# Kernel optimization log

Measured on AMD Instinct MI355X. Metric: run time of the kernel, lower is better.

Reference implementation:

```python
import jax, jax.numpy as jnp
import numpy as np

TOP_K = 8
N_GROUP = 8
TOPK_GROUP = 4
ROUTED_SCALE = 2.5


def setup_inputs() -> dict:
    key = jax.random.key(0)
    ks = jax.random.split(key, 7)
    T, H, E, I, SI = 4096, 1024, 32, 512, 2048
    W = 0.05  # weight scale to keep relu^2 activations sane
    return {
        "hidden_states": jax.random.normal(ks[0], (T, H), jnp.float32),
        "gate_w": jax.random.normal(ks[1], (E, H), jnp.float32) * W,
        "bias": jax.random.normal(ks[2], (E,), jnp.float32),
        "w_up": jax.random.normal(ks[3], (E, I, H), jnp.float32) * W,
        "w_down": jax.random.normal(ks[4], (E, H, I), jnp.float32) * W,
        "shared_up": jax.random.normal(ks[5], (SI, H), jnp.float32) * W,
        "shared_down": jax.random.normal(ks[6], (H, SI), jnp.float32) * W,
    }


def _grouped_topk_sigmoid(logits, bias):
    # vLLM grouped_topk with scoring_func='sigmoid' + e_score_correction_bias
    T, E = logits.shape
    scores = jax.nn.sigmoid(logits)                       # [T, E]
    sfc = scores + bias[None, :]                          # scores for choice
    g = sfc.reshape(T, N_GROUP, E // N_GROUP)
    group_scores = jnp.sum(jax.lax.top_k(g, 2)[0], -1)    # [T, G] sum of top-2
    grp_idx = jax.lax.top_k(group_scores, TOPK_GROUP)[1]  # [T, topk_group]
    gmask = jnp.zeros((T, N_GROUP), bool).at[jnp.arange(T)[:, None], grp_idx].set(True)
    emask = jnp.repeat(gmask, E // N_GROUP, axis=1)       # [T, E]
    masked = jnp.where(emask, sfc, -jnp.inf)
    topk_ids = jax.lax.top_k(masked, TOP_K)[1]            # [T, K]
    topk_w = jnp.take_along_axis(scores, topk_ids, axis=1)  # weights from raw scores
    topk_w = topk_w / jnp.sum(topk_w, axis=-1, keepdims=True)  # renormalize
    return topk_w, topk_ids


def reference(hidden_states, gate_w, bias, w_up, w_down, shared_up, shared_down):
    x = hidden_states
    T, H = x.shape
    E = gate_w.shape[0]
    # router (fp32 gate)
    logits = x.astype(jnp.float32) @ gate_w.T
    topk_w, topk_ids = _grouped_topk_sigmoid(logits, bias)
    # dense combine weights [T, E] (zero for unselected experts)
    gates = jnp.zeros((T, E), x.dtype).at[jnp.arange(T)[:, None], topk_ids].set(
        topk_w.astype(x.dtype))
    # routed experts: relu^2 MLP (no gating mul), combined with gate weights
    h = jnp.einsum('th,eih->tei', x, w_up)                # [T, E, I]
    h = jnp.square(jax.nn.relu(h))
    routed = jnp.einsum('tei,te,ehi->th', h, gates, w_down)
    # shared expert (same relu^2 MLP)
    s = jnp.square(jax.nn.relu(x @ shared_up.T)) @ shared_down.T
    return routed * ROUTED_SCALE + s
```

## Files before the change

kernel.cpp:

```cpp
#include <hip/hip_runtime.h>
#include <hip/hip_bf16.h>


typedef _Float16 h8 __attribute__((ext_vector_type(8)));
typedef _Float16 h4 __attribute__((ext_vector_type(4)));
typedef float f4 __attribute__((ext_vector_type(4)));

#define T_TOK 4096
#define HDIM  1024
#define NEXP  32
#define IDIM  512
#define SIDIM 2048
#define TOPK  8
#define MAXTILES 288

__device__ __forceinline__ void gload16(const void* g, void* l) {
    __builtin_amdgcn_global_load_lds(
        (const __attribute__((address_space(1))) void*)g,
        (__attribute__((address_space(3))) void*)l, 16, 0, 0);
}

__global__ void cvt_kernel(const float* __restrict__ in, _Float16* __restrict__ o, int n4) {
    int i = blockIdx.x * 256 + threadIdx.x;
    if (i < n4) {
        float4 v = reinterpret_cast<const float4*>(in)[i];
        h4 h; h[0] = (_Float16)v.x; h[1] = (_Float16)v.y; h[2] = (_Float16)v.z; h[3] = (_Float16)v.w;
        reinterpret_cast<h4*>(o)[i] = h;
    }
}

__global__ __launch_bounds__(256) void logits_kernel(
    const float* __restrict__ x, const float* __restrict__ gw,
    double* __restrict__ logits) {
    const int t0  = blockIdx.x * 16;
    const int tid = threadIdx.x;
    __shared__ double xS[16][66];
    __shared__ double gS[32][65];
    const int e  = tid & 31;
    const int tg = tid >> 5;
    const int tA = tg * 2, tB = tg * 2 + 1;
    double acc0 = 0.0, acc1 = 0.0;

    for (int kc = 0; kc < HDIM; kc += 64) {
        {
            int r = tid >> 4, c0 = (tid & 15) * 4;
            float4 v = *reinterpret_cast<const float4*>(x + (size_t)(t0 + r) * HDIM + kc + c0);
            xS[r][c0]     = (double)v.x;
            xS[r][c0 + 1] = (double)v.y;
            xS[r][c0 + 2] = (double)v.z;
            xS[r][c0 + 3] = (double)v.w;
        }
        {
            int r = tid >> 3, c0 = (tid & 7) * 8;
            const float* gp = gw + (size_t)r * HDIM + kc + c0;
            float4 v0 = *reinterpret_cast<const float4*>(gp);
            float4 v1 = *reinterpret_cast<const float4*>(gp + 4);
            gS[r][c0]     = (double)v0.x;
            gS[r][c0 + 1] = (double)v0.y;
            gS[r][c0 + 2] = (double)v0.z;
            gS[r][c0 + 3] = (double)v0.w;
            gS[r][c0 + 4] = (double)v1.x;
            gS[r][c0 + 5] = (double)v1.y;
            gS[r][c0 + 6] = (double)v1.z;
            gS[r][c0 + 7] = (double)v1.w;
        }
        __syncthreads();
#pragma unroll
        for (int k = 0; k < 64; ++k) {
            double g = gS[e][k];
            acc0 = fma(g, xS[tA][k], acc0);
            acc1 = fma(g, xS[tB][k], acc1);
        }
        __syncthreads();
    }
    logits[(size_t)(t0 + tA) * NEXP + e] = acc0;
    logits[(size_t)(t0 + tB) * NEXP + e] = acc1;
}

__global__ __launch_bounds__(256) void select_kernel(
    const double* __restrict__ logits, const float* __restrict__ bias,
    int* __restrict__ topk_ids, float* __restrict__ topk_w) {
    const int wid  = threadIdx.x >> 6;
    const int lane = threadIdx.x & 63;
    const int t    = blockIdx.x * 4 + wid;

    __shared__ double s_s[4][32];
    __shared__ double s_sfc[4][32];
    if (lane < 32) {
        double acc = logits[(size_t)t * NEXP + lane];
        double sg = 1.0 / (1.0 + exp(-acc));
        s_s[wid][lane]   = sg;
        s_sfc[wid][lane] = sg + (double)bias[lane];
    }
    __syncthreads();

    if (lane == 0) {
        double gsc[8];
        for (int g = 0; g < 8; ++g) {
            double m1 = -1e300, m2 = -1e300;
            for (int j = 0; j < 4; ++j) {
                double v = s_sfc[wid][g * 4 + j];
                if (v > m1) { m2 = m1; m1 = v; } else if (v > m2) { m2 = v; }
            }
            gsc[g] = m1 + m2;
        }
        bool gsel[8] = {};
        for (int r = 0; r < 4; ++r) {
            int best = 0; double bv = -1e300;
            for (int g = 0; g < 8; ++g)
                if (!gsel[g] && gsc[g] > bv) { bv = gsc[g]; best = g; }
            gsel[best] = true;
        }
        bool esel[32];
        for (int i2 = 0; i2 < 32; ++i2) esel[i2] = false;
        int ids[8]; double wsum = 0.0;
        for (int r = 0; r < 8; ++r) {
            int best = 0; double bv = -1e300;
            for (int e2 = 0; e2 < 32; ++e2)
                if (gsel[e2 >> 2] && !esel[e2] && s_sfc[wid][e2] > bv) { bv = s_sfc[wid][e2]; best = e2; }
            esel[best] = true;
            ids[r] = best;
            wsum += s_s[wid][best];
        }
        for (int r = 0; r < 8; ++r) {
            topk_ids[t * TOPK + r] = ids[r];
            topk_w[t * TOPK + r] = (float)(s_s[wid][ids[r]] / wsum * 2.5);
        }
    }
}

__global__ void build_lists_kernel(const int* __restrict__ ids, const float* __restrict__ w,
                                   int* __restrict__ tok_list, float* __restrict__ wt_list,
                                   int* __restrict__ dest_list, int* __restrict__ counts) {
    const int e = blockIdx.x;
    const int lane = threadIdx.x;
    int base = 0;
    for (int t0 = 0; t0 < T_TOK; t0 += 64) {
        int t = t0 + lane;
        int found = -1;
#pragma unroll
        for (int k = 0; k < TOPK; ++k)
            if (ids[t * TOPK + k] == e) found = k;
        unsigned long long mask = __ballot(found >= 0);
        if (found >= 0) {
            int pos = base + __popcll(mask & ((1ull << lane) - 1ull));
            tok_list[e * T_TOK + pos]  = t;
            wt_list[e * T_TOK + pos]   = w[t * TOPK + found];
            dest_list[e * T_TOK + pos] = t * TOPK + found;
        }
        base += __popcll(mask);
    }
    if (lane == 0) counts[e] = base;
}

__global__ void scan_offsets_kernel(const int* __restrict__ counts, int* __restrict__ offsets,
                                    int* __restrict__ tmap) {
    if (threadIdx.x == 0) {
        int run = 0, nt = 0;
        for (int e = 0; e < NEXP; ++e) {
            offsets[e] = run;
            for (int m0 = 0; m0 < counts[e]; m0 += 128) {
                tmap[1 + 2 * nt] = e;
                tmap[2 + 2 * nt] = m0;
                ++nt;
            }
            run += counts[e];
        }
        offsets[NEXP] = run;
        tmap[0] = nt;
    }
}

template<int K>
__device__ __forceinline__ void gemm128(const _Float16* const (&aSrc)[4],
                                        const _Float16* const (&bSrc)[4],
                                        f4 (&acc)[4][4]) {
    __shared__ __attribute__((aligned(16))) _Float16 As[128 * 64];
    __shared__ __attribute__((aligned(16))) _Float16 Bs[128 * 64];
    const int tid  = threadIdx.x;
    const int w    = tid >> 6, lane = tid & 63;
    const int wm   = (w & 1) * 64, wn = (w >> 1) * 64;
    const int ra   = lane & 15, kq = lane >> 4;

    for (int kk = 0; kk < K; kk += 64) {
#pragma unroll
        for (int i = 0; i < 4; ++i) {
            gload16(aSrc[i] + kk, As + (size_t)(i * 256 + w * 64) * 8);
            gload16(bSrc[i] + kk, Bs + (size_t)(i * 256 + w * 64) * 8);
        }
        __syncthreads();
#pragma unroll
        for (int s = 0; s < 2; ++s) {
            h8 af[4], bf[4];
#pragma unroll
            for (int m = 0; m < 4; ++m) {
                int row = wm + m * 16 + ra;
                af[m] = *reinterpret_cast<const h8*>(As + row * 64 + (((s * 4 + kq) ^ (row & 7)) << 3));
            }
#pragma unroll
            for (int n = 0; n < 4; ++n) {
                int row = wn + n * 16 + ra;
                bf[n] = *reinterpret_cast<const h8*>(Bs + row * 64 + (((s * 4 + kq) ^ (row & 7)) << 3));
            }
#pragma unroll
            for (int m = 0; m < 4; ++m)
#pragma unroll
                for (int n = 0; n < 4; ++n)
                    acc[m][n] = __builtin_amdgcn_mfma_f32_16x16x32_f16(af[m], bf[n], acc[m][n], 0, 0, 0);
        }
        __syncthreads();
    }
}

__global__ __launch_bounds__(256) void up_routed_kernel(
    const _Float16* __restrict__ xh, const _Float16* __restrict__ whup,
    const int* __restrict__ tok_list, const float* __restrict__ wt_list,
    const int* __restrict__ counts, const int* __restrict__ offsets,
    const int* __restrict__ tmap, _Float16* __restrict__ hbuf) {
    const int ti = blockIdx.x;
    if (ti >= tmap[0]) return;
    const int e   = tmap[1 + 2 * ti];
    const int m0  = tmap[2 + 2 * ti];
    const int cnt = counts[e];
    const int n0   = blockIdx.y * 128;
    const int eoff = offsets[e];

    __shared__ int   tokS[128];
    __shared__ float wS[128];
    const int tid = threadIdx.x;
    if (tid < 128) {
        int row = m0 + tid;
        int cr  = row < cnt ? row : cnt - 1;
        tokS[tid] = tok_list[e * T_TOK + cr];
        wS[tid]   = row < cnt ? wt_list[e * T_TOK + row] : 0.f;
    }
    __syncthreads();

    const int sc = ((tid & 7) ^ ((tid >> 3) & 7)) << 3;
    const int r0 = tid >> 3;
    const _Float16* aSrc[4]; const _Float16* bSrc[4];
#pragma unroll
    for (int i = 0; i < 4; ++i) {
        aSrc[i] = xh + (size_t)tokS[i * 32 + r0] * HDIM + sc;
        bSrc[i] = whup + ((size_t)e * IDIM + n0 + i * 32 + r0) * HDIM + sc;
    }
    f4 acc[4][4] = {};
    gemm128<HDIM>(aSrc, bSrc, acc);

    const int w = tid >> 6, lane = tid & 63;
    const int wm = (w & 1) * 64, wn = (w >> 1) * 64;
    const int cq = lane >> 4, cc = lane & 15;
#pragma unroll
    for (int m = 0; m < 4; ++m)
#pragma unroll
    for (int r = 0; r < 4; ++r) {
        int orow = wm + m * 16 + cq * 4 + r;
        if (m0 + orow < cnt) {
            float g = wS[orow];
            size_t rb = (size_t)(eoff + m0 + orow) * IDIM + n0;
#pragma unroll
            for (int n = 0; n < 4; ++n) {
                float v = fmaxf(acc[m][n][r], 0.f);
                hbuf[rb + wn + n * 16 + cc] = (_Float16)(v * v * g);
            }
        }
    }
}

template<bool SLOT>
__global__ __launch_bounds__(256) void down_routed_kernel(
    const _Float16* __restrict__ hbuf, const _Float16* __restrict__ whdown,
    const int* __restrict__ dest_list, const int* __restrict__ counts,
    const int* __restrict__ offsets, const int* __restrict__ tmap,
    _Float16* __restrict__ slotout, float* __restrict__ out) {
    const int ti = blockIdx.x;
    if (ti >= tmap[0]) return;
    const int e   = tmap[1 + 2 * ti];
    const int m0  = tmap[2 + 2 * ti];
    const int cnt = counts[e];
    const int n0   = blockIdx.y * 128;
    const int eoff = offsets[e];

    __shared__ int dS[128];
    const int tid = threadIdx.x;
    if (tid < 128) {
        int row = m0 + tid;
        dS[tid] = dest_list[e * T_TOK + (row < cnt ? row : cnt - 1)];
    }

    const int sc = ((tid & 7) ^ ((tid >> 3) & 7)) << 3;
    const int r0 = tid >> 3;
    const _Float16* aSrc[4]; const _Float16* bSrc[4];
#pragma unroll
    for (int i = 0; i < 4; ++i) {
        int row = m0 + i * 32 + r0;
        int cr  = row < cnt ? row : cnt - 1;
        aSrc[i] = hbuf + (size_t)(eoff + cr) * IDIM + sc;
        bSrc[i] = whdown + ((size_t)e * HDIM + n0 + i * 32 + r0) * IDIM + sc;
    }
    f4 acc[4][4] = {};
    gemm128<IDIM>(aSrc, bSrc, acc);

    const int w = tid >> 6, lane = tid & 63;
    const int wm = (w & 1) * 64, wn = (w >> 1) * 64;
    const int cq = lane >> 4, cc = lane & 15;
#pragma unroll
    for (int m = 0; m < 4; ++m)
#pragma unroll
    for (int r = 0; r < 4; ++r) {
        int orow = wm + m * 16 + cq * 4 + r;
        if (m0 + orow < cnt) {
            int d = dS[orow];
            if (SLOT) {
                size_t rb = (size_t)d * HDIM + n0;
#pragma unroll
                for (int n = 0; n < 4; ++n)
                    slotout[rb + wn + n * 16 + cc] = (_Float16)acc[m][n][r];
            } else {
                size_t rb = (size_t)(d >> 3) * HDIM + n0;
#pragma unroll
                for (int n = 0; n < 4; ++n)
                    atomicAdd(&out[rb + wn + n * 16 + cc], acc[m][n][r]);
            }
        }
    }
}

__global__ __launch_bounds__(256) void up_shared_kernel(
    const _Float16* __restrict__ xh, const _Float16* __restrict__ shup,
    _Float16* __restrict__ sh) {
    const int m0 = blockIdx.y * 128;
    const int n0 = blockIdx.x * 128;
    const int tid = threadIdx.x;
    const int sc = ((tid & 7) ^ ((tid >> 3) & 7)) << 3;
    const int r0 = tid >> 3;
    const _Float16* aSrc[4]; const _Float16* bSrc[4];
#pragma unroll
    for (int i = 0; i < 4; ++i) {
        aSrc[i] = xh + (size_t)(m0 + i * 32 + r0) * HDIM + sc;
        bSrc[i] = shup + (size_t)(n0 + i * 32 + r0) * HDIM + sc;
    }
    f4 acc[4][4] = {};
    gemm128<HDIM>(aSrc, bSrc, acc);

    const int w = tid >> 6, lane = tid & 63;
    const int wm = (w & 1) * 64, wn = (w >> 1) * 64;
    const int cq = lane >> 4, cc = lane & 15;
#pragma unroll
    for (int m = 0; m < 4; ++m)
#pragma unroll
    for (int r = 0; r < 4; ++r) {
        int orow = wm + m * 16 + cq * 4 + r;
        size_t rb = (size_t)(m0 + orow) * SIDIM + n0;
#pragma unroll
        for (int n = 0; n < 4; ++n) {
            float v = fmaxf(acc[m][n][r], 0.f);
            sh[rb + wn + n * 16 + cc] = (_Float16)(v * v);
        }
    }
}

__global__ __launch_bounds__(256) void down_shared_kernel(
    const _Float16* __restrict__ sh, const _Float16* __restrict__ shdown,
    float* __restrict__ out) {
    const int m0 = blockIdx.y * 128;
    const int n0 = blockIdx.x * 128;
    const int tid = threadIdx.x;
    const int sc = ((tid & 7) ^ ((tid >> 3) & 7)) << 3;
    const int r0 = tid >> 3;
    const _Float16* aSrc[4]; const _Float16* bSrc[4];
#pragma unroll
    for (int i = 0; i < 4; ++i) {
        aSrc[i] = sh + (size_t)(m0 + i * 32 + r0) * SIDIM + sc;
        bSrc[i] = shdown + (size_t)(n0 + i * 32 + r0) * SIDIM + sc;
    }
    f4 acc[4][4] = {};
    gemm128<SIDIM>(aSrc, bSrc, acc);

    const int w = tid >> 6, lane = tid & 63;
    const int wm = (w & 1) * 64, wn = (w >> 1) * 64;
    const int cq = lane >> 4, cc = lane & 15;
#pragma unroll
    for (int m = 0; m < 4; ++m)
#pragma unroll
    for (int r = 0; r < 4; ++r) {
        int orow = wm + m * 16 + cq * 4 + r;
        size_t rb = (size_t)(m0 + orow) * HDIM + n0;
#pragma unroll
        for (int n = 0; n < 4; ++n)
            out[rb + wn + n * 16 + cc] = acc[m][n][r];
    }
}

__global__ __launch_bounds__(256) void combine_kernel(
    const _Float16* __restrict__ slotout, float* __restrict__ out) {
    int gi = blockIdx.x * 256 + threadIdx.x;
    int t  = gi >> 8;
    int c4 = gi & 255;
    size_t ob = (size_t)t * HDIM + c4 * 4;
    float4 v = *reinterpret_cast<const float4*>(out + ob);
    float s0 = v.x, s1 = v.y, s2 = v.z, s3 = v.w;
#pragma unroll
    for (int k = 0; k < TOPK; ++k) {
        h4 p = *reinterpret_cast<const h4*>(slotout + ((size_t)(t * TOPK + k)) * HDIM + c4 * 4);
        s0 += (float)p[0]; s1 += (float)p[1]; s2 += (float)p[2]; s3 += (float)p[3];
    }
    float4 r = {s0, s1, s2, s3};
    *reinterpret_cast<float4*>(out + ob) = r;
}

extern "C" void kernel_launch(void* const* d_in, const int* in_sizes, int n_in,
                              void* d_out, int out_size, void* d_ws, size_t ws_size,
                              hipStream_t stream) {
    const float* x     = (const float*)d_in[0];
    const float* gw    = (const float*)d_in[1];
    const float* bias  = (const float*)d_in[2];
    const float* wup   = (const float*)d_in[3];
    const float* wdown = (const float*)d_in[4];
    const float* sup   = (const float*)d_in[5];
    const float* sdown = (const float*)d_in[6];
    float* out = (float*)d_out;

    char* ws = (char*)d_ws;
    size_t off = 0;
    auto take = [&](size_t bytes) {
        char* p = ws + off;
        off = (off + bytes + 255) & ~(size_t)255;
        return p;
    };
    _Float16* xh      = (_Float16*)take((size_t)T_TOK * HDIM * 2);
    _Float16* whup    = (_Float16*)take((size_t)NEXP * IDIM * HDIM * 2);
    _Float16* whdown  = (_Float16*)take((size_t)NEXP * HDIM * IDIM * 2);
    _Float16* shupW   = (_Float16*)take((size_t)SIDIM * HDIM * 2);
    _Float16* shdownW = (_Float16*)take((size_t)HDIM * SIDIM * 2);
    _Float16* sh      = (_Float16*)take((size_t)T_TOK * SIDIM * 2);
    _Float16* hbuf    = (_Float16*)take((size_t)T_TOK * TOPK * IDIM * 2);
    double* logits   = (double*)take((size_t)T_TOK * NEXP * 8);
    int*   ids       = (int*)take((size_t)T_TOK * TOPK * 4);
    float* tw        = (float*)take((size_t)T_TOK * TOPK * 4);
    int*   tok_list  = (int*)take((size_t)NEXP * T_TOK * 4);
    float* wt_list   = (float*)take((size_t)NEXP * T_TOK * 4);
    int*   dest_list = (int*)take((size_t)NEXP * T_TOK * 4);
    int*   counts    = (int*)take(NEXP * 4);
    int*   offsets   = (int*)take((NEXP + 1) * 4);
    int*   tmap      = (int*)take((1 + 2 * MAXTILES) * 4);
    _Float16* slotout = (_Float16*)take((size_t)T_TOK * TOPK * HDIM * 2);
    const bool use_slot = off <= ws_size;

    logits_kernel<<<T_TOK / 16, 256, 0, stream>>>(x, gw, logits);
    select_kernel<<<T_TOK / 4, 256, 0, stream>>>(logits, bias, ids, tw);
    build_lists_kernel<<<NEXP, 64, 0, stream>>>(ids, tw, tok_list, wt_list, dest_list, counts);
    scan_offsets_kernel<<<1, 64, 0, stream>>>(counts, offsets, tmap);

    cvt_kernel<<<(T_TOK * HDIM / 4 + 255) / 256, 256, 0, stream>>>(x, xh, T_TOK * HDIM / 4);
    cvt_kernel<<<(NEXP * IDIM * HDIM / 4 + 255) / 256, 256, 0, stream>>>(wup, whup, NEXP * IDIM * HDIM / 4);
    cvt_kernel<<<(NEXP * HDIM * IDIM / 4 + 255) / 256, 256, 0, stream>>>(wdown, whdown, NEXP * HDIM * IDIM / 4);
    cvt_kernel<<<(SIDIM * HDIM / 4 + 255) / 256, 256, 0, stream>>>(sup, shupW, SIDIM * HDIM / 4);
    cvt_kernel<<<(HDIM * SIDIM / 4 + 255) / 256, 256, 0, stream>>>(sdown, shdownW, HDIM * SIDIM / 4);

    up_routed_kernel<<<dim3(MAXTILES, IDIM / 128), 256, 0, stream>>>(
        xh, whup, tok_list, wt_list, counts, offsets, tmap, hbuf);
    up_shared_kernel<<<dim3(SIDIM / 128, T_TOK / 128), 256, 0, stream>>>(xh, shupW, sh);
    down_shared_kernel<<<dim3(HDIM / 128, T_TOK / 128), 256, 0, stream>>>(sh, shdownW, out);

    if (use_slot) {
        down_routed_kernel<true><<<dim3(MAXTILES, HDIM / 128), 256, 0, stream>>>(
            hbuf, whdown, dest_list, counts, offsets, tmap, slotout, out);
        combine_kernel<<<T_TOK * HDIM / 4 / 256, 256, 0, stream>>>(slotout, out);
    } else {
        down_routed_kernel<false><<<dim3(MAXTILES, HDIM / 128), 256, 0, stream>>>(
            hbuf, whdown, dest_list, counts, offsets, tmap, slotout, out);
    }
}
```

Baseline: 365.8 us.

## Use double-buffered 256x128 GEMM tiles and fuse router, conversion and combine kernels

Adds a gemm256 path with 512-thread blocks, 256-row tiles, LDS double buffering with explicit vmcnt waits and setprio around MFMA, and uses it for the routed up/down and shared-up GEMMs. The logits and selection kernels are merged so the double logits buffer goes away, the five fp32-to-fp16 conversions become one grid-stride launch, and the slot combine is folded into the shared-down epilogue. This targets launch overhead, extra memory round trips and exposed load latency. The larger tiles waste more rows on partial expert tiles and raise LDS and register pressure.

Result: faster. 347.5 us (-5.0%).

```diff
diff --git a/kernel.cpp b/kernel.cpp
--- a/kernel.cpp
+++ b/kernel.cpp
@@ -12,7 +12,7 @@
 #define IDIM  512
 #define SIDIM 2048
 #define TOPK  8
-#define MAXTILES 288
+#define MAXT256 160
 
 __device__ __forceinline__ void gload16(const void* g, void* l) {
     __builtin_amdgcn_global_load_lds(
@@ -20,22 +20,39 @@
         (__attribute__((address_space(3))) void*)l, 16, 0, 0);
 }
 
-__global__ void cvt_kernel(const float* __restrict__ in, _Float16* __restrict__ o, int n4) {
-    int i = blockIdx.x * 256 + threadIdx.x;
-    if (i < n4) {
-        float4 v = reinterpret_cast<const float4*>(in)[i];
+__global__ __launch_bounds__(256) void cvt_all_kernel(
+    const float* __restrict__ sA, _Float16* __restrict__ dA, int nA,
+    const float* __restrict__ sB, _Float16* __restrict__ dB, int nB,
+    const float* __restrict__ sC, _Float16* __restrict__ dC, int nC,
+    const float* __restrict__ sD, _Float16* __restrict__ dD, int nD,
+    const float* __restrict__ sE, _Float16* __restrict__ dE, int nE) {
+    const int total = nA + nB + nC + nD + nE;
+    for (int gi = blockIdx.x * 256 + threadIdx.x; gi < total; gi += gridDim.x * 256) {
+        const float* s; _Float16* d; int i = gi;
+        if (i < nA) { s = sA; d = dA; }
+        else { i -= nA;
+        if (i < nB) { s = sB; d = dB; }
+        else { i -= nB;
+        if (i < nC) { s = sC; d = dC; }
+        else { i -= nC;
+        if (i < nD) { s = sD; d = dD; }
+        else { i -= nD; s = sE; d = dE; } } } }
+        float4 v = reinterpret_cast<const float4*>(s)[i];
         h4 h; h[0] = (_Float16)v.x; h[1] = (_Float16)v.y; h[2] = (_Float16)v.z; h[3] = (_Float16)v.w;
-        reinterpret_cast<h4*>(o)[i] = h;
-    }
-}
-
-__global__ __launch_bounds__(256) void logits_kernel(
+        reinterpret_cast<h4*>(d)[i] = h;
+    }
+}
+
+__global__ __launch_bounds__(256) void logits_select_kernel(
     const float* __restrict__ x, const float* __restrict__ gw,
-    double* __restrict__ logits) {
+    const float* __restrict__ bias, int* __restrict__ topk_ids,
+    float* __restrict__ topk_w) {
     const int t0  = blockIdx.x * 16;
     const int tid = threadIdx.x;
     __shared__ double xS[16][66];
     __shared__ double gS[32][65];
+    __shared__ double sS[16][33];
+    __shared__ double sfcS[16][33];
     const int e  = tid & 31;
     const int tg = tid >> 5;
     const int tA = tg * 2, tB = tg * 2 + 1;
@@ -73,33 +90,22 @@
         }
         __syncthreads();
     }
-    logits[(size_t)(t0 + tA) * NEXP + e] = acc0;
-    logits[(size_t)(t0 + tB) * NEXP + e] = acc1;
-}
-
-__global__ __launch_bounds__(256) void select_kernel(
-    const double* __restrict__ logits, const float* __restrict__ bias,
-    int* __restrict__ topk_ids, float* __restrict__ topk_w) {
-    const int wid  = threadIdx.x >> 6;
-    const int lane = threadIdx.x & 63;
-    const int t    = blockIdx.x * 4 + wid;
-
-    __shared__ double s_s[4][32];
-    __shared__ double s_sfc[4][32];
-    if (lane < 32) {
-        double acc = logits[(size_t)t * NEXP + lane];
-        double sg = 1.0 / (1.0 + exp(-acc));
-        s_s[wid][lane]   = sg;
-        s_sfc[wid][lane] = sg + (double)bias[lane];
+    {
+        double s0 = 1.0 / (1.0 + exp(-acc0));
+        double s1 = 1.0 / (1.0 + exp(-acc1));
+        double b = (double)bias[e];
+        sS[tA][e] = s0;  sfcS[tA][e] = s0 + b;
+        sS[tB][e] = s1;  sfcS[tB][e] = s1 + b;
     }
     __syncthreads();
 
-    if (lane == 0) {
+    if (tid < 16) {
+        const int t = t0 + tid;
         double gsc[8];
         for (int g = 0; g < 8; ++g) {
             double m1 = -1e300, m2 = -1e300;
             for (int j = 0; j < 4; ++j) {
-                double v = s_sfc[wid][g * 4 + j];
+                double v = sfcS[tid][g * 4 + j];
                 if (v > m1) { m2 = m1; m1 = v; } else if (v > m2) { m2 = v; }
             }
             gsc[g] = m1 + m2;
@@ -117,14 +123,14 @@
         for (int r = 0; r < 8; ++r) {
             int best = 0; double bv = -1e300;
             for (int e2 = 0; e2 < 32; ++e2)
-                if (gsel[e2 >> 2] && !esel[e2] && s_sfc[wid][e2] > bv) { bv = s_sfc[wid][e2]; best = e2; }
+                if (gsel[e2 >> 2] && !esel[e2] && sfcS[tid][e2] > bv) { bv = sfcS[tid][e2]; best = e2; }
             esel[best] = true;
             ids[r] = best;
-            wsum += s_s[wid][best];
+            wsum += sS[tid][best];
         }
         for (int r = 0; r < 8; ++r) {
             topk_ids[t * TOPK + r] = ids[r];
-            topk_w[t * TOPK + r] = (float)(s_s[wid][ids[r]] / wsum * 2.5);
+            topk_w[t * TOPK + r] = (float)(sS[tid][ids[r]] / wsum * 2.5);
         }
     }
 }
@@ -159,7 +165,7 @@
         int run = 0, nt = 0;
         for (int e = 0; e < NEXP; ++e) {
             offsets[e] = run;
-            for (int m0 = 0; m0 < counts[e]; m0 += 128) {
+            for (int m0 = 0; m0 < counts[e]; m0 += 256) {
                 tmap[1 + 2 * nt] = e;
                 tmap[2 + 2 * nt] = m0;
                 ++nt;
@@ -172,47 +178,79 @@
 }
 
 template<int K>
-__device__ __forceinline__ void gemm128(const _Float16* const (&aSrc)[4],
-                                        const _Float16* const (&bSrc)[4],
+__device__ __forceinline__ void gemm256(const _Float16* const (&aP)[4],
+                                        const _Float16* const (&bP)[2],
                                         f4 (&acc)[4][4]) {
-    __shared__ __attribute__((aligned(16))) _Float16 As[128 * 64];
-    __shared__ __attribute__((aligned(16))) _Float16 Bs[128 * 64];
+    __shared__ __attribute__((aligned(16))) _Float16 As[2][256 * 64];
+    __shared__ __attribute__((aligned(16))) _Float16 Bs[2][128 * 64];
     const int tid  = threadIdx.x;
     const int w    = tid >> 6, lane = tid & 63;
-    const int wm   = (w & 1) * 64, wn = (w >> 1) * 64;
+    const int wm   = (w >> 1) * 64;
+    const int wn   = (w & 1) * 64;
     const int ra   = lane & 15, kq = lane >> 4;
-
-    for (int kk = 0; kk < K; kk += 64) {
-#pragma unroll
-        for (int i = 0; i < 4; ++i) {
-            gload16(aSrc[i] + kk, As + (size_t)(i * 256 + w * 64) * 8);
-            gload16(bSrc[i] + kk, Bs + (size_t)(i * 256 + w * 64) * 8);
-        }
-        __syncthreads();
-#pragma unroll
-        for (int s = 0; s < 2; ++s) {
-            h8 af[4], bf[4];
-#pragma unroll
-            for (int m = 0; m < 4; ++m) {
-                int row = wm + m * 16 + ra;
-                af[m] = *reinterpret_cast<const h8*>(As + row * 64 + (((s * 4 + kq) ^ (row & 7)) << 3));
-            }
-#pragma unroll
-            for (int n = 0; n < 4; ++n) {
+    const int nt   = K / 64;
+
+#pragma unroll
+    for (int i = 0; i < 4; ++i)
+        gload16(aP[i], &As[0][(i * 64 + w * 8) * 64]);
+#pragma unroll
+    for (int j = 0; j < 2; ++j)
+        gload16(bP[j], &Bs[0][(j * 64 + w * 8) * 64]);
+
+    for (int t = 0; t < nt; ++t) {
+        const int cur = t & 1;
+        if (t + 1 < nt) {
+#pragma unroll
+            for (int i = 0; i < 4; ++i)
+                gload16(aP[i] + (t + 1) * 64, &As[cur ^ 1][(i * 64 + w * 8) * 64]);
+#pragma unroll
+            for (int j = 0; j < 2; ++j)
+                gload16(bP[j] + (t + 1) * 64, &Bs[cur ^ 1][(j * 64 + w * 8) * 64]);
+            asm volatile("s_waitcnt vmcnt(6)" ::: "memory");
+        } else {
+            asm volatile("s_waitcnt vmcnt(0)" ::: "memory");
+        }
+        __builtin_amdgcn_s_barrier();
+        asm volatile("" ::: "memory");
+
+        h8 bF[4][2];
+#pragma unroll
+        for (int n = 0; n < 4; ++n)
+#pragma unroll
+            for (int ks = 0; ks < 2; ++ks) {
                 int row = wn + n * 16 + ra;
-                bf[n] = *reinterpret_cast<const h8*>(Bs + row * 64 + (((s * 4 + kq) ^ (row & 7)) << 3));
-            }
-#pragma unroll
-            for (int m = 0; m < 4; ++m)
-#pragma unroll
-                for (int n = 0; n < 4; ++n)
-                    acc[m][n] = __builtin_amdgcn_mfma_f32_16x16x32_f16(af[m], bf[n], acc[m][n], 0, 0, 0);
-        }
-        __syncthreads();
-    }
-}
-
-__global__ __launch_bounds__(256) void up_routed_kernel(
+                bF[n][ks] = *reinterpret_cast<const h8*>(
+                    &Bs[cur][row * 64 + (((ks * 4 + kq) ^ (ra & 7)) << 3)]);
+            }
+#pragma unroll
+        for (int mh = 0; mh < 2; ++mh) {
+            h8 aF[2][2];
+#pragma unroll
+            for (int mq = 0; mq < 2; ++mq)
+#pragma unroll
+                for (int ks = 0; ks < 2; ++ks) {
+                    int row = wm + mh * 32 + mq * 16 + ra;
+                    aF[mq][ks] = *reinterpret_cast<const h8*>(
+                        &As[cur][row * 64 + (((ks * 4 + kq) ^ (ra & 7)) << 3)]);
+                }
+            __builtin_amdgcn_s_setprio(1);
+#pragma unroll
+            for (int ks = 0; ks < 2; ++ks)
+#pragma unroll
+                for (int mq = 0; mq < 2; ++mq)
+#pragma unroll
+                    for (int n = 0; n < 4; ++n)
+                        acc[mh * 2 + mq][n] = __builtin_amdgcn_mfma_f32_16x16x32_f16(
+                            aF[mq][ks], bF[n][ks], acc[mh * 2 + mq][n], 0, 0, 0);
+            __builtin_amdgcn_s_setprio(0);
+        }
+        asm volatile("" ::: "memory");
+        __builtin_amdgcn_s_barrier();
+        asm volatile("" ::: "memory");
+    }
+}
+
+__global__ __launch_bounds__(512, 2) void up_routed_kernel(
     const _Float16* __restrict__ xh, const _Float16* __restrict__ whup,
     const int* __restrict__ tok_list, const float* __restrict__ wt_list,
     const int* __restrict__ counts, const int* __restrict__ offsets,
@@ -225,10 +263,10 @@
     const int n0   = blockIdx.y * 128;
     const int eoff = offsets[e];
 
-    __shared__ int   tokS[128];
-    __shared__ float wS[128];
+    __shared__ int   tokS[256];
+    __shared__ float wS[256];
     const int tid = threadIdx.x;
-    if (tid < 128) {
+    if (tid < 256) {
         int row = m0 + tid;
         int cr  = row < cnt ? row : cnt - 1;
         tokS[tid] = tok_list[e * T_TOK + cr];
@@ -236,25 +274,27 @@
     }
     __syncthreads();
 
-    const int sc = ((tid & 7) ^ ((tid >> 3) & 7)) << 3;
-    const int r0 = tid >> 3;
-    const _Float16* aSrc[4]; const _Float16* bSrc[4];
-#pragma unroll
-    for (int i = 0; i < 4; ++i) {
-        aSrc[i] = xh + (size_t)tokS[i * 32 + r0] * HDIM + sc;
-        bSrc[i] = whup + ((size_t)e * IDIM + n0 + i * 32 + r0) * HDIM + sc;
-    }
+    const int w = tid >> 6, lane = tid & 63;
+    const int swz = ((lane & 7) ^ (lane >> 3)) << 3;
+    const int rr  = w * 8 + (lane >> 3);
+    const _Float16* aP[4]; const _Float16* bP[2];
+#pragma unroll
+    for (int i = 0; i < 4; ++i)
+        aP[i] = xh + (size_t)tokS[i * 64 + rr] * HDIM + swz;
+#pragma unroll
+    for (int j = 0; j < 2; ++j)
+        bP[j] = whup + ((size_t)e * IDIM + n0 + j * 64 + rr) * HDIM + swz;
+
     f4 acc[4][4] = {};
-    gemm128<HDIM>(aSrc, bSrc, acc);
-
-    const int w = tid >> 6, lane = tid & 63;
-    const int wm = (w & 1) * 64, wn = (w >> 1) * 64;
-    const int cq = lane >> 4, cc = lane & 15;
+    gemm256<HDIM>(aP, bP, acc);
+
+    const int wm = (w >> 1) * 64, wn = (w & 1) * 64;
+    const int kq = lane >> 4, cc = lane & 15;
 #pragma unroll
     for (int m = 0; m < 4; ++m)
 #pragma unroll
     for (int r = 0; r < 4; ++r) {
-        int orow = wm + m * 16 + cq * 4 + r;
+        int orow = wm + m * 16 + kq * 4 + r;
         if (m0 + orow < cnt) {
             float g = wS[orow];
             size_t rb = (size_t)(eoff + m0 + orow) * IDIM + n0;
@@ -268,7 +308,7 @@
 }
 
 template<bool SLOT>
-__global__ __launch_bounds__(256) void down_routed_kernel(
+__global__ __launch_bounds__(512, 2) void down_routed_kernel(
     const _Float16* __restrict__ hbuf, const _Float16* __restrict__ whdown,
     const int* __restrict__ dest_list, const int* __restrict__ counts,
     const int* __restrict__ offsets, const int* __restrict__ tmap,
@@ -281,34 +321,38 @@
     const int n0   = blockIdx.y * 128;
     const int eoff = offsets[e];
 
-    __shared__ int dS[128];
+    __shared__ int dS[256];
     const int tid = threadIdx.x;
-    if (tid < 128) {
+    if (tid < 256) {
         int row = m0 + tid;
         dS[tid] = dest_list[e * T_TOK + (row < cnt ? row : cnt - 1)];
     }
-
-    const int sc = ((tid & 7) ^ ((tid >> 3) & 7)) << 3;
-    const int r0 = tid >> 3;
-    const _Float16* aSrc[4]; const _Float16* bSrc[4];
+    __syncthreads();
+
+    const int w = tid >> 6, lane = tid & 63;
+    const int swz = ((lane & 7) ^ (lane >> 3)) << 3;
+    const int rr  = w * 8 + (lane >> 3);
+    const _Float16* aP[4]; const _Float16* bP[2];
 #pragma unroll
     for (int i = 0; i < 4; ++i) {
-        int row = m0 + i * 32 + r0;
+        int row = m0 + i * 64 + rr;
         int cr  = row < cnt ? row : cnt - 1;
-        aSrc[i] = hbuf + (size_t)(eoff + cr) * IDIM + sc;
-        bSrc[i] = whdown + ((size_t)e * HDIM + n0 + i * 32 + r0) * IDIM + sc;
-    }
+        aP[i] = hbuf + (size_t)(eoff + cr) * IDIM + swz;
+    }
+#pragma unroll
+    for (int j = 0; j < 2; ++j)
+        bP[j] = whdown + ((size_t)e * HDIM + n0 + j * 64 + rr) * IDIM + swz;
+
     f4 acc[4][4] = {};
-    gemm128<IDIM>(aSrc, bSrc, acc);
-
-    const int w = tid >> 6, lane = tid & 63;
-    const int wm = (w & 1) * 64, wn = (w >> 1) * 64;
-    const int cq = lane >> 4, cc = lane & 15;
+    gemm256<IDIM>(aP, bP, acc);
+
+    const int wm = (w >> 1) * 64, wn = (w & 1) * 64;
+    const int kq = lane >> 4, cc = lane & 15;
 #pragma unroll
     for (int m = 0; m < 4; ++m)
 #pragma unroll
     for (int r = 0; r < 4; ++r) {
-        int orow = wm + m * 16 + cq * 4 + r;
+        int orow = wm + m * 16 + kq * 4 + r;
         if (m0 + orow < cnt) {
             int d = dS[orow];
             if (SLOT) {
@@ -326,9 +370,87 @@
     }
 }
 
-__global__ __launch_bounds__(256) void up_shared_kernel(
+__global__ __launch_bounds__(512, 2) void up_shared_kernel(
     const _Float16* __restrict__ xh, const _Float16* __restrict__ shup,
     _Float16* __restrict__ sh) {
+    const int m0 = blockIdx.x * 256;
+    const int n0 = blockIdx.y * 128;
+    const int tid = threadIdx.x;
+    const int w = tid >> 6, lane = tid & 63;
+    const int swz = ((lane & 7) ^ (lane >> 3)) << 3;
+    const int rr  = w * 8 + (lane >> 3);
+    const _Float16* aP[4]; const _Float16* bP[2];
+#pragma unroll
+    for (int i = 0; i < 4; ++i)
+        aP[i] = xh + (size_t)(m0 + i * 64 + rr) * HDIM + swz;
+#pragma unroll
+    for (int j = 0; j < 2; ++j)
+        bP[j] = shup + (size_t)(n0 + j * 64 + rr) * HDIM + swz;
+
+    f4 acc[4][4] = {};
+    gemm256<HDIM>(aP, bP, acc);
+
+    const int wm = (w >> 1) * 64, wn = (w & 1) * 64;
+    const int kq = lane >> 4, cc = lane & 15;
+#pragma unroll
+    for (int m = 0; m < 4; ++m)
+#pragma unroll
+    for (int r = 0; r < 4; ++r) {
+        int orow = wm + m * 16 + kq * 4 + r;
+        size_t rb = (size_t)(m0 + orow) * SIDIM + n0;
+#pragma unroll
+        for (int n = 0; n < 4; ++n) {
+            float v = fmaxf(acc[m][n][r], 0.f);
+            sh[rb + wn + n * 16 + cc] = (_Float16)(v * v);
+        }
+    }
+}
+
+template<int K>
+__device__ __forceinline__ void gemm128(const _Float16* const (&aSrc)[4],
+                                        const _Float16* const (&bSrc)[4],
+                                        f4 (&acc)[4][4]) {
+    __shared__ __attribute__((aligned(16))) _Float16 As[128 * 64];
+    __shared__ __attribute__((aligned(16))) _Float16 Bs[128 * 64];
+    const int tid  = threadIdx.x;
+    const int w    = tid >> 6, lane = tid & 63;
+    const int wm   = (w & 1) * 64, wn = (w >> 1) * 64;
+    const int ra   = lane & 15, kq = lane >> 4;
+
+    for (int kk = 0; kk < K; kk += 64) {
+#pragma unroll
+        for (int i = 0; i < 4; ++i) {
+            gload16(aSrc[i] + kk, As + (size_t)(i * 256 + w * 64) * 8);
+            gload16(bSrc[i] + kk, Bs + (size_t)(i * 256 + w * 64) * 8);
+        }
+        __syncthreads();
+#pragma unroll
+        for (int s = 0; s < 2; ++s) {
+            h8 af[4], bf[4];
+#pragma unroll
+            for (int m = 0; m < 4; ++m) {
+                int row = wm + m * 16 + ra;
+                af[m] = *reinterpret_cast<const h8*>(As + row * 64 + (((s * 4 + kq) ^ (row & 7)) << 3));
+            }
+#pragma unroll
+            for (int n = 0; n < 4; ++n) {
+                int row = wn + n * 16 + ra;
+                bf[n] = *reinterpret_cast<const h8*>(Bs + row * 64 + (((s * 4 + kq) ^ (row & 7)) << 3));
+            }
+#pragma unroll
+            for (int m = 0; m < 4; ++m)
+#pragma unroll
+                for (int n = 0; n < 4; ++n)
+                    acc[m][n] = __builtin_amdgcn_mfma_f32_16x16x32_f16(af[m], bf[n], acc[m][n], 0, 0, 0);
+        }
+        __syncthreads();
+    }
+}
+
+template<bool COMB>
+__global__ __launch_bounds__(256) void down_shared_kernel(
+    const _Float16* __restrict__ sh, const _Float16* __restrict__ shdown,
+    const _Float16* __restrict__ slotout, float* __restrict__ out) {
     const int m0 = blockIdx.y * 128;
     const int n0 = blockIdx.x * 128;
     const int tid = threadIdx.x;
@@ -337,11 +459,11 @@
     const _Float16* aSrc[4]; const _Float16* bSrc[4];
 #pragma unroll
     for (int i = 0; i < 4; ++i) {
-        aSrc[i] = xh + (size_t)(m0 + i * 32 + r0) * HDIM + sc;
-        bSrc[i] = shup + (size_t)(n0 + i * 32 + r0) * HDIM + sc;
+        aSrc[i] = sh + (size_t)(m0 + i * 32 + r0) * SIDIM + sc;
+        bSrc[i] = shdown + (size_t)(n0 + i * 32 + r0) * SIDIM + sc;
     }
     f4 acc[4][4] = {};
-    gemm128<HDIM>(aSrc, bSrc, acc);
+    gemm128<SIDIM>(aSrc, bSrc, acc);
 
     const int w = tid >> 6, lane = tid & 63;
     const int wm = (w & 1) * 64, wn = (w >> 1) * 64;
@@ -351,62 +473,20 @@
 #pragma unroll
     for (int r = 0; r < 4; ++r) {
         int orow = wm + m * 16 + cq * 4 + r;
-        size_t rb = (size_t)(m0 + orow) * SIDIM + n0;
+        size_t trow = (size_t)(m0 + orow);
 #pragma unroll
         for (int n = 0; n < 4; ++n) {
-            float v = fmaxf(acc[m][n][r], 0.f);
-            sh[rb + wn + n * 16 + cc] = (_Float16)(v * v);
-        }
-    }
-}
-
-__global__ __launch_bounds__(256) void down_shared_kernel(
-    const _Float16* __restrict__ sh, const _Float16* __restrict__ shdown,
-    float* __restrict__ out) {
-    const int m0 = blockIdx.y * 128;
-    const int n0 = blockIdx.x * 128;
-    const int tid = threadIdx.x;
-    const int sc = ((tid & 7) ^ ((tid >> 3) & 7)) << 3;
-    const int r0 = tid >> 3;
-    const _Float16* aSrc[4]; const _Float16* bSrc[4];
-#pragma unroll
-    for (int i = 0; i < 4; ++i) {
-        aSrc[i] = sh + (size_t)(m0 + i * 32 + r0) * SIDIM + sc;
-        bSrc[i] = shdown + (size_t)(n0 + i * 32 + r0) * SIDIM + sc;
-    }
-    f4 acc[4][4] = {};
-    gemm128<SIDIM>(aSrc, bSrc, acc);
-
-    const int w = tid >> 6, lane = tid & 63;
-    const int wm = (w & 1) * 64, wn = (w >> 1) * 64;
-    const int cq = lane >> 4, cc = lane & 15;
-#pragma unroll
-    for (int m = 0; m < 4; ++m)
-#pragma unroll
-    for (int r = 0; r < 4; ++r) {
-        int orow = wm + m * 16 + cq * 4 + r;
-        size_t rb = (size_t)(m0 + orow) * HDIM + n0;
-#pragma unroll
-        for (int n = 0; n < 4; ++n)
-            out[rb + wn + n * 16 + cc] = acc[m][n][r];
-    }
-}
-
-__global__ __launch_bounds__(256) void combine_kernel(
-    const _Float16* __restrict__ slotout, float* __restrict__ out) {
-    int gi = blockIdx.x * 256 + threadIdx.x;
-    int t  = gi >> 8;
-    int c4 = gi & 255;
-    size_t ob = (size_t)t * HDIM + c4 * 4;
-    float4 v = *reinterpret_cast<const float4*>(out + ob);
-    float s0 = v.x, s1 = v.y, s2 = v.z, s3 = v.w;
-#pragma unroll
-    for (int k = 0; k < TOPK; ++k) {
-        h4 p = *reinterpret_cast<const h4*>(slotout + ((size_t)(t * TOPK + k)) * HDIM + c4 * 4);
-        s0 += (float)p[0]; s1 += (float)p[1]; s2 += (float)p[2]; s3 += (float)p[3];
-    }
-    float4 r = {s0, s1, s2, s3};
-    *reinterpret_cast<float4*>(out + ob) = r;
+            int col = n0 + wn + n * 16 + cc;
+            float v = acc[m][n][r];
+            if (COMB) {
+                const _Float16* sp = slotout + trow * TOPK * HDIM + col;
+#pragma unroll
+                for (int k = 0; k < TOPK; ++k)
+                    v += (float)sp[(size_t)k * HDIM];
+            }
+            out[trow * HDIM + col] = v;
+        }
+    }
 }
 
 extern "C" void kernel_launch(void* const* d_in, const int* in_sizes, int n_in,
@@ -435,7 +515,6 @@
     _Float16* shdownW = (_Float16*)take((size_t)HDIM * SIDIM * 2);
     _Float16* sh      = (_Float16*)take((size_t)T_TOK * SIDIM * 2);
     _Float16* hbuf    = (_Float16*)take((size_t)T_TOK * TOPK * IDIM * 2);
-    double* logits   = (double*)take((size_t)T_TOK * NEXP * 8);
     int*   ids       = (int*)take((size_t)T_TOK * TOPK * 4);
     float* tw        = (float*)take((size_t)T_TOK * TOPK * 4);
     int*   tok_list  = (int*)take((size_t)NEXP * T_TOK * 4);
@@ -443,32 +522,34 @@
     int*   dest_list = (int*)take((size_t)NEXP * T_TOK * 4);
     int*   counts    = (int*)take(NEXP * 4);
     int*   offsets   = (int*)take((NEXP + 1) * 4);
-    int*   tmap      = (int*)take((1 + 2 * MAXTILES) * 4);
+    int*   tmap      = (int*)take((1 + 2 * MAXT256) * 4);
     _Float16* slotout = (_Float16*)take((size_t)T_TOK * TOPK * HDIM * 2);
     const bool use_slot = off <= ws_size;
 
-    logits_kernel<<<T_TOK / 16, 256, 0, stream>>>(x, gw, logits);
-    select_kernel<<<T_TOK / 4, 256, 0, stream>>>(logits, bias, ids, tw);
+    logits_select_kernel<<<T_TOK / 16, 256, 0, stream>>>(x, gw, bias, ids, tw);
     build_lists_kernel<<<NEXP, 64, 0, stream>>>(ids, tw, tok_list, wt_list, dest_list, counts);
     scan_offsets_kernel<<<1, 64, 0, stream>>>(counts, offsets, tmap);
 
-    cvt_kernel<<<(T_TOK * HDIM / 4 + 255) / 256, 256, 0, stream>>>(x, xh, T_TOK * HDIM / 4);
-    cvt_kernel<<<(NEXP * IDIM * HDIM / 4 + 255) / 256, 256, 0, stream>>>(wup, whup, NEXP * IDIM * HDIM / 4);
-    cvt_kernel<<<(NEXP * HDIM * IDIM / 4 + 255) / 256, 256, 0, stream>>>(wdown, whdown, NEXP * HDIM * IDIM / 4);
-    cvt_kernel<<<(SIDIM * HDIM / 4 + 255) / 256, 256, 0, stream>>>(sup, shupW, SIDIM * HDIM / 4);
-    cvt_kernel<<<(HDIM * SIDIM / 4 + 255) / 256, 256, 0, stream>>>(sdown, shdownW, HDIM * SIDIM / 4);
-
-    up_routed_kernel<<<dim3(MAXTILES, IDIM / 128), 256, 0, stream>>>(
+    cvt_all_kernel<<<2048, 256, 0, stream>>>(
+        x, xh, T_TOK * HDIM / 4,
+        wup, whup, NEXP * IDIM * HDIM / 4,
+        wdown, whdown, NEXP * HDIM * IDIM / 4,
+        sup, shupW, SIDIM * HDIM / 4,
+        sdown, shdownW, HDIM * SIDIM / 4);
+
+    up_routed_kernel<<<dim3(MAXT256, IDIM / 128), 512, 0, stream>>>(
         xh, whup, tok_list, wt_list, counts, offsets, tmap, hbuf);
-    up_shared_kernel<<<dim3(SIDIM / 128, T_TOK / 128), 256, 0, stream>>>(xh, shupW, sh);
-    down_shared_kernel<<<dim3(HDIM / 128, T_TOK / 128), 256, 0, stream>>>(sh, shdownW, out);
+    up_shared_kernel<<<dim3(T_TOK / 256, SIDIM / 128), 512, 0, stream>>>(xh, shupW, sh);
 
     if (use_slot) {
-        down_routed_kernel<true><<<dim3(MAXTILES, HDIM / 128), 256, 0, stream>>>(
+        down_routed_kernel<true><<<dim3(MAXT256, HDIM / 128), 512, 0, stream>>>(
             hbuf, whdown, dest_list, counts, offsets, tmap, slotout, out);
-        combine_kernel<<<T_TOK * HDIM / 4 / 256, 256, 0, stream>>>(slotout, out);
+        down_shared_kernel<true><<<dim3(HDIM / 128, T_TOK / 128), 256, 0, stream>>>(
+            sh, shdownW, slotout, out);
     } else {
-        down_routed_kernel<false><<<dim3(MAXTILES, HDIM / 128), 256, 0, stream>>>(
+        down_shared_kernel<false><<<dim3(HDIM / 128, T_TOK / 128), 256, 0, stream>>>(
+            sh, shdownW, slotout, out);
+        down_routed_kernel<false><<<dim3(MAXT256, HDIM / 128), 512, 0, stream>>>(
             hbuf, whdown, dest_list, counts, offsets, tmap, slotout, out);
     }
 }
```
